# Kernel optimization log

Measured on AMD Instinct MI355X. Metric: run time of the kernel, lower is better.

Reference implementation:

```python
import jax, jax.numpy as jnp
import numpy as np

D = 256      # hidden_size
H = 4        # num_attention_heads
DH = D // H  # dim per head = 64
L = 4        # num_hidden_layers
M = 266      # nb_features = int(64 * ln(64))
S = 4096     # seq len / max_position_embeddings
B = 4
LN_EPS = 1e-12


def layer_norm(x, g, b, eps=LN_EPS):
    mu = jnp.mean(x, -1, keepdims=True)
    var = jnp.var(x, -1, keepdims=True)
    return (x - mu) / jnp.sqrt(var + eps) * g + b


def softmax_kernel(x, proj, is_query, eps=1e-4):
    # x: [b,h,s,d], proj: [m,d] -> phi(x): [b,h,s,m] (FAVOR+ positive features)
    d = x.shape[-1]
    m = proj.shape[0]
    dn = d ** -0.25
    ratio = m ** -0.5
    dash = jnp.einsum('bhsd,md->bhsm', x, proj) * dn
    diag = jnp.sum(x * x, -1, keepdims=True) * 0.5 * (dn * dn)
    if is_query:
        stab = jnp.max(dash, -1, keepdims=True)  # per-query stabilizer
    else:
        stab = jnp.max(dash)  # global stabilizer for keys
    return ratio * (jnp.exp(dash - diag - stab) + eps)


def favor_attention(x, proj, Wq, bq, Wk, bk, Wv, bv, Wo, bo):
    b, s, d = x.shape
    split = lambda t: t.reshape(b, s, H, DH).transpose(0, 2, 1, 3)  # [b,h,s,dh]
    q = split(x @ Wq + bq)
    k = split(x @ Wk + bk)
    v = split(x @ Wv + bv)
    qp = softmax_kernel(q, proj, True)   # [b,h,s,m]
    kp = softmax_kernel(k, proj, False)  # [b,h,s,m]
    ksum = kp.sum(axis=2)                                  # [b,h,m]
    d_inv = 1.0 / jnp.einsum('bhsm,bhm->bhs', qp, ksum)    # normalizer
    ctx = jnp.einsum('bhsm,bhse->bhme', kp, v)             # [b,h,m,dh]
    out = jnp.einsum('bhsm,bhme,bhs->bhse', qp, ctx, d_inv)
    out = out.transpose(0, 2, 1, 3).reshape(b, s, d)
    return out @ Wo + bo


def _forward(input_embs, attention_mask, pos_emb, ln_g, ln_b, proj,
             Wq, bq, Wk, bk, Wv, bv, Wo, bo, ln1_g, ln1_b,
             W1, b1, W2, b2, ln2_g, ln2_b, p1_w, p1_b, p2_w, p2_b):
    b, s, d = input_embs.shape
    x = input_embs + pos_emb[:s][None]
    x = layer_norm(x, ln_g, ln_b)  # dropout is identity at eval
    for i in range(L):
        x = x + favor_attention(layer_norm(x, ln1_g[i], ln1_b[i]), proj[i],
                                Wq[i], bq[i], Wk[i], bk[i], Wv[i], bv[i], Wo[i], bo[i])
        h = layer_norm(x, ln2_g[i], ln2_b[i])
        x = x + (jax.nn.gelu(h @ W1[i] + b1[i]) @ W2[i] + b2[i])
    # AttentionPooling
    e = jnp.tanh(x @ p1_w + p1_b)
    alpha = jnp.exp(e @ p2_w + p2_b)            # [b,s,1]
    alpha = alpha * attention_mask[..., None]
    alpha = alpha / (jnp.sum(alpha, 1, keepdims=True) + 1e-8)
    return jnp.einsum('bsd,bs->bd', x, alpha[..., 0])


def setup_inputs() -> dict:
    key = jax.random.key(0)
    ks = iter(jax.random.split(key, 32))
    std = 0.02
    nrm = lambda shape: jax.random.normal(next(ks), shape, jnp.float32)
    return {
        'input_embs': nrm((B, S, D)),
        'attention_mask': jnp.ones((B, S), jnp.float32),
        'pos_emb': nrm((S, D)) * std,
        'ln_g': jnp.ones((D,), jnp.float32), 'ln_b': jnp.zeros((D,), jnp.float32),
        'proj': nrm((L, M, DH)),
        'Wq': nrm((L, D, D)) * std, 'bq': jnp.zeros((L, D), jnp.float32),
        'Wk': nrm((L, D, D)) * std, 'bk': jnp.zeros((L, D), jnp.float32),
        'Wv': nrm((L, D, D)) * std, 'bv': jnp.zeros((L, D), jnp.float32),
        'Wo': nrm((L, D, D)) * std, 'bo': jnp.zeros((L, D), jnp.float32),
        'ln1_g': jnp.ones((L, D), jnp.float32), 'ln1_b': jnp.zeros((L, D), jnp.float32),
        'W1': nrm((L, D, 4 * D)) * std, 'b1': jnp.zeros((L, 4 * D), jnp.float32),
        'W2': nrm((L, 4 * D, D)) * std, 'b2': jnp.zeros((L, D), jnp.float32),
        'ln2_g': jnp.ones((L, D), jnp.float32), 'ln2_b': jnp.zeros((L, D), jnp.float32),
        'p1_w': nrm((D, D)) * std, 'p1_b': jnp.zeros((D,), jnp.float32),
        'p2_w': nrm((D, 1)) * std, 'p2_b': jnp.zeros((1,), jnp.float32),
    }


def reference(input_embs, attention_mask, pos_emb, ln_g, ln_b, proj,
              Wq, bq, Wk, bk, Wv, bv, Wo, bo, ln1_g, ln1_b,
              W1, b1, W2, b2, ln2_g, ln2_b, p1_w, p1_b, p2_w, p2_b):
    return _forward(input_embs, attention_mask, pos_emb, ln_g, ln_b, proj,
                    Wq, bq, Wk, bk, Wv, bv, Wo, bo, ln1_g, ln1_b,
                    W1, b1, W2, b2, ln2_g, ln2_b, p1_w, p1_b, p2_w, p2_b)
```

## Files before the change

### kernel.cpp

```cpp
#include <hip/hip_runtime.h>
#include <math.h>


#define WS_ALIGN(x) (((x) + 255) & ~(size_t)255)

#define DN 0.35355339059327373f
#define DIAGC 0.0625f
#define RATIO 0.06131393394849658f
#define FEPS 1e-4f

typedef __attribute__((__ext_vector_type__(8))) __bf16 bf16x8;
typedef __attribute__((__ext_vector_type__(4))) float f32x4;

__device__ __forceinline__ float wredsum(float v) {
    v += __shfl_xor(v, 32); v += __shfl_xor(v, 16); v += __shfl_xor(v, 8);
    v += __shfl_xor(v, 4);  v += __shfl_xor(v, 2);  v += __shfl_xor(v, 1);
    return v;
}
__device__ __forceinline__ float wredmax(float v) {
    v = fmaxf(v, __shfl_xor(v, 32)); v = fmaxf(v, __shfl_xor(v, 16));
    v = fmaxf(v, __shfl_xor(v, 8));  v = fmaxf(v, __shfl_xor(v, 4));
    v = fmaxf(v, __shfl_xor(v, 2));  v = fmaxf(v, __shfl_xor(v, 1));
    return v;
}

__device__ __forceinline__ unsigned short f2bf(float f) {
    unsigned u = __builtin_bit_cast(unsigned, f);
    return (unsigned short)((u + 0x7fffu + ((u >> 16) & 1u)) >> 16);
}
__device__ __forceinline__ float blo(unsigned x) { return __builtin_bit_cast(float, x << 16); }
__device__ __forceinline__ float bhi(unsigned x) { return __builtin_bit_cast(float, x & 0xffff0000u); }
__device__ __forceinline__ float sumsq8(uint4 u) {
    float s = 0.f;
    s += blo(u.x)*blo(u.x) + bhi(u.x)*bhi(u.x);
    s += blo(u.y)*blo(u.y) + bhi(u.y)*bhi(u.y);
    s += blo(u.z)*blo(u.z) + bhi(u.z)*bhi(u.z);
    s += blo(u.w)*blo(u.w) + bhi(u.w)*bhi(u.w);
    return s;
}
__device__ __forceinline__ unsigned pack2(float a, float b) {
    return (unsigned)f2bf(a) | ((unsigned)f2bf(b) << 16);
}

__device__ __forceinline__ void gload_lds16(const unsigned short* g, unsigned short* lds) {
    __builtin_amdgcn_global_load_lds(
        (const __attribute__((address_space(1))) unsigned int*)g,
        (__attribute__((address_space(3))) unsigned int*)lds, 16, 0, 0);
}

__global__ __launch_bounds__(256) void add_ln2_kernel(
    const float* __restrict__ in, const float* __restrict__ pos,
    const float* __restrict__ g0, const float* __restrict__ b0,
    const float* __restrict__ g1, const float* __restrict__ b1,
    float* __restrict__ xout, unsigned short* __restrict__ hout)
{
    int row = blockIdx.x, t = threadIdx.x;
    __shared__ float sred[4];
    float v = in[(size_t)row * 256 + t] + pos[(size_t)(row & 4095) * 256 + t];
    float s = wredsum(v);
    if ((t & 63) == 0) sred[t >> 6] = s;
    __syncthreads();
    float mean = (sred[0] + sred[1] + sred[2] + sred[3]) * (1.0f / 256.0f);
    float d = v - mean;
    __syncthreads();
    float sq = wredsum(d * d);
    if ((t & 63) == 0) sred[t >> 6] = sq;
    __syncthreads();
    float var = (sred[0] + sred[1] + sred[2] + sred[3]) * (1.0f / 256.0f);
    float y1 = d * rsqrtf(var + 1e-12f) * g0[t] + b0[t];
    xout[(size_t)row * 256 + t] = y1;
    __syncthreads();
    float s1 = wredsum(y1);
    if ((t & 63) == 0) sred[t >> 6] = s1;
    __syncthreads();
    float mean1 = (sred[0] + sred[1] + sred[2] + sred[3]) * (1.0f / 256.0f);
    float d1 = y1 - mean1;
    __syncthreads();
    float sq1 = wredsum(d1 * d1);
    if ((t & 63) == 0) sred[t >> 6] = sq1;
    __syncthreads();
    float var1 = (sred[0] + sred[1] + sred[2] + sred[3]) * (1.0f / 256.0f);
    hout[(size_t)row * 256 + t] = f2bf(d1 * rsqrtf(var1 + 1e-12f) * g1[t] + b1[t]);
}

__global__ __launch_bounds__(256) void cast_transpose_kernel(
    const float* __restrict__ in, unsigned short* __restrict__ out, int R, int C)
{
    __shared__ float tile[32][33];
    size_t zo = (size_t)blockIdx.z * R * C;
    int c0 = blockIdx.x * 32, r0 = blockIdx.y * 32;
    int t = threadIdx.x, tc = t & 31, tr = t >> 5;
#pragma unroll
    for (int j = 0; j < 4; j++)
        tile[tr + j * 8][tc] = in[zo + (size_t)(r0 + tr + j * 8) * C + c0 + tc];
    __syncthreads();
#pragma unroll
    for (int j = 0; j < 4; j++) {
        int cc = tr + j * 8, rr = tc;
        out[zo + (size_t)(c0 + cc) * R + r0 + rr] = f2bf(tile[rr][cc]);
    }
}

__global__ __launch_bounds__(256) void cast_transpose4_kernel(
    const float* __restrict__ i0, const float* __restrict__ i1,
    const float* __restrict__ i2, const float* __restrict__ i3,
    unsigned short* __restrict__ o0, unsigned short* __restrict__ o1,
    unsigned short* __restrict__ o2, unsigned short* __restrict__ o3)
{
    __shared__ float tile[32][33];
    int z = blockIdx.z;
    int which = z >> 2, layer = z & 3;
    const float* in = (which == 0) ? i0 : (which == 1) ? i1 : (which == 2) ? i2 : i3;
    unsigned short* out = (which == 0) ? o0 : (which == 1) ? o1 : (which == 2) ? o2 : o3;
    size_t zo = (size_t)layer * 65536;
    int c0 = blockIdx.x * 32, r0 = blockIdx.y * 32;
    int t = threadIdx.x, tc = t & 31, tr = t >> 5;
#pragma unroll
    for (int j = 0; j < 4; j++)
        tile[tr + j * 8][tc] = in[zo + (size_t)(r0 + tr + j * 8) * 256 + c0 + tc];
    __syncthreads();
#pragma unroll
    for (int j = 0; j < 4; j++) {
        int cc = tr + j * 8, rr = tc;
        out[zo + (size_t)(c0 + cc) * 256 + r0 + rr] = f2bf(tile[rr][cc]);
    }
}

__global__ __launch_bounds__(256) void cast_row_kernel(
    const float4* __restrict__ in, ushort4* __restrict__ out, int n4)
{
    int i = blockIdx.x * 256 + threadIdx.x;
    if (i >= n4) return;
    float4 v = in[i];
    ushort4 o; o.x = f2bf(v.x); o.y = f2bf(v.y); o.z = f2bf(v.z); o.w = f2bf(v.w);
    out[i] = o;
}

__global__ __launch_bounds__(256) void ctx_cast_kernel(
    const float* __restrict__ ctxT, unsigned short* __restrict__ ctxbf)
{
    int idx = blockIdx.x * 256 + threadIdx.x;
    int row = idx / 36;
    int c = idx - row * 36;
    int m = c * 8;
    uint4 pk = {0, 0, 0, 0};
    if (m < 272) {
        const float* src = ctxT + (size_t)row * 272 + m;
        float4 f0 = *(const float4*)(src);
        float4 f1 = *(const float4*)(src + 4);
        pk.x = pack2(f0.x, f0.y); pk.y = pack2(f0.z, f0.w);
        pk.z = pack2(f1.x, f1.y); pk.w = pack2(f1.z, f1.w);
    }
    *(uint4*)(ctxbf + (size_t)row * 288 + c * 8) = pk;
}

__global__ __launch_bounds__(256) void qkv_kernel(
    const unsigned short* __restrict__ A,
    const unsigned short* __restrict__ Wqt, const unsigned short* __restrict__ Wkt,
    const unsigned short* __restrict__ Wvt,
    const float* __restrict__ bq, const float* __restrict__ bk, const float* __restrict__ bv,
    unsigned short* __restrict__ qbf, unsigned short* __restrict__ kbf,
    unsigned short* __restrict__ vT)
{
    __shared__ uint4 As[128][5];
    __shared__ uint4 Bs[64][5];
    const int K = 256;
    int t = threadIdx.x;
    int bm = blockIdx.y * 128, bn = blockIdx.x * 64;
    int grp = bn >> 8, lbn = bn & 255;
    const unsigned short* Bt = (grp == 0) ? Wqt : (grp == 1) ? Wkt : Wvt;
    const float* bias = (grp == 0) ? bq : (grp == 1) ? bk : bv;
    int w = t >> 6, l = t & 63, lm16 = l & 15, quad = l >> 4;
    int ar = t >> 1, ak = (t & 1) * 16;
    int br = t >> 2, bk2 = (t & 3) * 8;
    const unsigned short* Ab = A + (size_t)(bm + ar) * K + ak;
    const unsigned short* Bb = Bt + (size_t)(lbn + br) * K + bk2;
    f32x4 acc[2][4] = {};
    for (int k0 = 0; k0 < K; k0 += 32) {
        uint4 a0 = *(const uint4*)(Ab + k0);
        uint4 a1 = *(const uint4*)(Ab + k0 + 8);
        uint4 b0 = *(const uint4*)(Bb + k0);
        __syncthreads();
        As[ar][(ak >> 3)] = a0; As[ar][(ak >> 3) + 1] = a1;
        Bs[br][bk2 >> 3] = b0;
        __syncthreads();
        bf16x8 af[2], bfr[4];
        af[0] = *(const bf16x8*)&As[w * 32 + lm16][quad];
        af[1] = *(const bf16x8*)&As[w * 32 + 16 + lm16][quad];
#pragma unroll
        for (int j = 0; j < 4; j++) bfr[j] = *(const bf16x8*)&Bs[j * 16 + lm16][quad];
#pragma unroll
        for (int i = 0; i < 2; i++)
#pragma unroll
            for (int j = 0; j < 4; j++)
                acc[i][j] = __builtin_amdgcn_mfma_f32_16x16x32_bf16(af[i], bfr[j], acc[i][j], 0, 0, 0);
    }
#pragma unroll
    for (int i = 0; i < 2; i++)
#pragma unroll
        for (int j = 0; j < 4; j++) {
            int lcol = lbn + j * 16 + lm16;
            float bs = bias[lcol];
            int h = lcol >> 6, e = lcol & 63;
#pragma unroll
            for (int r = 0; r < 4; r++) {
                int row = bm + w * 32 + i * 16 + quad * 4 + r;
                int b = row >> 12, s = row & 4095;
                float v = acc[i][j][r] + bs;
                if (grp == 0)
                    qbf[((size_t)((b << 2) + h) * 4096 + s) * 64 + e] = f2bf(v);
                else if (grp == 1)
                    kbf[((size_t)((b << 2) + h) * 4096 + s) * 64 + e] = f2bf(v);
                else
                    vT[((size_t)((b << 2) + h) * 64 + e) * 4096 + s] = f2bf(v);
            }
        }
}

__global__ __launch_bounds__(256) void ffn1_kernel(
    const unsigned short* __restrict__ A, const unsigned short* __restrict__ Bt,
    const float* __restrict__ bias, unsigned short* __restrict__ Cb, int N, int K)
{
    __shared__ uint4 As[128][5];
    __shared__ uint4 Bs[64][5];
    int t = threadIdx.x;
    int bm = blockIdx.y * 128, bn = blockIdx.x * 64;
    int w = t >> 6, l = t & 63, lm16 = l & 15, quad = l >> 4;
    int ar = t >> 1, ak = (t & 1) * 16;
    int br = t >> 2, bk = (t & 3) * 8;
    const unsigned short* Ab = A + (size_t)(bm + ar) * K + ak;
    const unsigned short* Bb = Bt + (size_t)(bn + br) * K + bk;
    f32x4 acc[2][4] = {};
    for (int k0 = 0; k0 < K; k0 += 32) {
        uint4 a0 = *(const uint4*)(Ab + k0);
        uint4 a1 = *(const uint4*)(Ab + k0 + 8);
        uint4 b0 = *(const uint4*)(Bb + k0);
        __syncthreads();
        As[ar][(ak >> 3)] = a0; As[ar][(ak >> 3) + 1] = a1;
        Bs[br][bk >> 3] = b0;
        __syncthreads();
        bf16x8 af[2], bfr[4];
        af[0] = *(const bf16x8*)&As[w * 32 + lm16][quad];
        af[1] = *(const bf16x8*)&As[w * 32 + 16 + lm16][quad];
#pragma unroll
        for (int j = 0; j < 4; j++) bfr[j] = *(const bf16x8*)&Bs[j * 16 + lm16][quad];
#pragma unroll
        for (int i = 0; i < 2; i++)
#pragma unroll
            for (int j = 0; j < 4; j++)
                acc[i][j] = __builtin_amdgcn_mfma_f32_16x16x32_bf16(af[i], bfr[j], acc[i][j], 0, 0, 0);
    }
#pragma unroll
    for (int i = 0; i < 2; i++)
#pragma unroll
        for (int j = 0; j < 4; j++) {
            int col = bn + j * 16 + lm16;
            float bsv = bias[col];
#pragma unroll
            for (int r = 0; r < 4; r++) {
                int row = bm + w * 32 + i * 16 + quad * 4 + r;
                float v = acc[i][j][r] + bsv;
                float inner = 0.7978845608028654f * (v + 0.044715f * v * v * v);
                float gl = 0.5f * v * (1.0f + tanhf(inner));
                Cb[(size_t)row * N + col] = f2bf(gl);
            }
        }
}

template <int EPI>
__global__ __launch_bounds__(512) void gemm_fullrow_kernel(
    const unsigned short* __restrict__ A, const unsigned short* __restrict__ Bt,
    const float* __restrict__ bias, float* __restrict__ xio,
    const float* __restrict__ lng, const float* __restrict__ lnb,
    unsigned short* __restrict__ outb,
    const float* __restrict__ p2w, const float* __restrict__ p2b,
    const float* __restrict__ mask, float* __restrict__ alphab, int K)
{
    __shared__ uint4 As4[64][5];
    __shared__ uint4 Bs4[256][5];
    __shared__ float red[8][64];
    int t = threadIdx.x;
    int bm = blockIdx.x * 64;
    int w = t >> 6, l = t & 63, lm16 = l & 15, quad = l >> 4;
    int br = t >> 2, bj = t & 3;
    f32x4 acc[4][2] = {};
    for (int k0 = 0; k0 < K; k0 += 32) {
        uint4 a = {0, 0, 0, 0};
        if (t < 256) a = *(const uint4*)(A + (size_t)(bm + (t >> 2)) * K + k0 + (t & 3) * 8);
        uint4 b0 = *(const uint4*)(Bt + (size_t)br * K + k0 + bj * 8);
        uint4 b1 = *(const uint4*)(Bt + (size_t)(br + 128) * K + k0 + bj * 8);
        __syncthreads();
        if (t < 256) As4[t >> 2][t & 3] = a;
        Bs4[br][bj] = b0;
        Bs4[br + 128][bj] = b1;
        __syncthreads();
        bf16x8 af[4], bfv[2];
#pragma unroll
        for (int i = 0; i < 4; i++) af[i] = *(const bf16x8*)&As4[i * 16 + lm16][quad];
#pragma unroll
        for (int j = 0; j < 2; j++) bfv[j] = *(const bf16x8*)&Bs4[w * 32 + j * 16 + lm16][quad];
#pragma unroll
        for (int i = 0; i < 4; i++)
#pragma unroll
            for (int j = 0; j < 2; j++)
                acc[i][j] = __builtin_amdgcn_mfma_f32_16x16x32_bf16(af[i], bfv[j], acc[i][j], 0, 0, 0);
    }
    int colbase = w * 32;
    if (EPI == 2) {
        float rs[4][4] = {};
#pragma unroll
        for (int j = 0; j < 2; j++) {
            int col = colbase + j * 16 + lm16;
            float bs = bias[col], pw = p2w[col];
#pragma unroll
            for (int i = 0; i < 4; i++)
#pragma unroll
                for (int r = 0; r < 4; r++)
                    rs[i][r] += tanhf(acc[i][j][r] + bs) * pw;
        }
#pragma unroll
        for (int m2 = 1; m2 <= 8; m2 <<= 1)
#pragma unroll
            for (int i = 0; i < 4; i++)
#pragma unroll
                for (int r = 0; r < 4; r++) rs[i][r] += __shfl_xor(rs[i][r], m2);
        __syncthreads();
        if (lm16 == 0) {
#pragma unroll
            for (int i = 0; i < 4; i++)
#pragma unroll
                for (int r = 0; r < 4; r++) red[w][i * 16 + quad * 4 + r] = rs[i][r];
        }
        __syncthreads();
        if (t < 64) {
            float sc = p2b[0];
#pragma unroll
            for (int ww = 0; ww < 8; ww++) sc += red[ww][t];
            int row = bm + t;
            alphab[row] = expf(sc) * mask[row];
        }
        return;
    }
    float rs[4][4] = {};
#pragma unroll
    for (int j = 0; j < 2; j++) {
        int col = colbase + j * 16 + lm16;
        float bs = bias[col];
#pragma unroll
        for (int i = 0; i < 4; i++)
#pragma unroll
            for (int r = 0; r < 4; r++) {
                int row = bm + i * 16 + quad * 4 + r;
                float v = acc[i][j][r] + bs + xio[(size_t)row * 256 + col];
                acc[i][j][r] = v;
                rs[i][r] += v;
            }
    }
    float mean[4][4], rstd[4][4];
    if (EPI == 0) {
#pragma unroll
        for (int m2 = 1; m2 <= 8; m2 <<= 1)
#pragma unroll
            for (int i = 0; i < 4; i++)
#pragma unroll
                for (int r = 0; r < 4; r++) rs[i][r] += __shfl_xor(rs[i][r], m2);
        __syncthreads();
        if (lm16 == 0) {
#pragma unroll
            for (int i = 0; i < 4; i++)
#pragma unroll
                for (int r = 0; r < 4; r++) red[w][i * 16 + quad * 4 + r] = rs[i][r];
        }
        __syncthreads();
        float vs[4][4] = {};
#pragma unroll
        for (int i = 0; i < 4; i++)
#pragma unroll
            for (int r = 0; r < 4; r++) {
                int rr = i * 16 + quad * 4 + r;
                float s = 0.f;
#pragma unroll
                for (int ww = 0; ww < 8; ww++) s += red[ww][rr];
                mean[i][r] = s * (1.0f / 256.0f);
            }
#pragma unroll
        for (int j = 0; j < 2; j++)
#pragma unroll
            for (int i = 0; i < 4; i++)
#pragma unroll
                for (int r = 0; r < 4; r++) {
                    float d = acc[i][j][r] - mean[i][r];
                    vs[i][r] += d * d;
                }
#pragma unroll
        for (int m2 = 1; m2 <= 8; m2 <<= 1)
#pragma unroll
            for (int i = 0; i < 4; i++)
#pragma unroll
                for (int r = 0; r < 4; r++) vs[i][r] += __shfl_xor(vs[i][r], m2);
        __syncthreads();
        if (lm16 == 0) {
#pragma unroll
            for (int i = 0; i < 4; i++)
#pragma unroll
                for (int r = 0; r < 4; r++) red[w][i * 16 + quad * 4 + r] = vs[i][r];
        }
        __syncthreads();
#pragma unroll
        for (int i = 0; i < 4; i++)
#pragma unroll
            for (int r = 0; r < 4; r++) {
                int rr = i * 16 + quad * 4 + r;
                float s = 0.f;
#pragma unroll
                for (int ww = 0; ww < 8; ww++) s += red[ww][rr];
                rstd[i][r] = rsqrtf(s * (1.0f / 256.0f) + 1e-12f);
            }
    }
#pragma unroll
    for (int j = 0; j < 2; j++) {
        int col = colbase + j * 16 + lm16;
        float g  = (EPI == 0) ? lng[col] : 0.f;
        float bb = (EPI == 0) ? lnb[col] : 0.f;
#pragma unroll
        for (int i = 0; i < 4; i++)
#pragma unroll
            for (int r = 0; r < 4; r++) {
                int row = bm + i * 16 + quad * 4 + r;
                float v = acc[i][j][r];
                xio[(size_t)row * 256 + col] = v;
                float y = (EPI == 0) ? ((v - mean[i][r]) * rstd[i][r] * g + bb) : v;
                outb[(size_t)row * 256 + col] = f2bf(y);
            }
    }
}

#define ZERO_FLOATS 282880
__global__ __launch_bounds__(256) void phi_kmax_kernel(
    const unsigned short* __restrict__ kbf, const unsigned short* __restrict__ projbf,
    float* __restrict__ pmax, float* __restrict__ zbase)
{
    __shared__ uint4 As[64][9];
    __shared__ uint4 Bs[272][9];
    __shared__ float diag_s[64];
    __shared__ float sred[4];
    int t = threadIdx.x;
    int s0 = blockIdx.x * 64;
    int bh = blockIdx.y;
    {
        int bid = blockIdx.y * 64 + blockIdx.x;
        for (int i = bid * 256 + t; i < ZERO_FLOATS; i += 1024 * 256) zbase[i] = 0.f;
    }
    {
        int arow = t >> 2, akoff = (t & 3) * 16;
        const uint4* ga = (const uint4*)(kbf + ((size_t)bh * 4096 + s0 + arow) * 64 + akoff);
        uint4 u0 = ga[0], u1 = ga[1];
        As[arow][(akoff >> 3)] = u0; As[arow][(akoff >> 3) + 1] = u1;
        float ss = sumsq8(u0) + sumsq8(u1);
        ss += __shfl_xor(ss, 1); ss += __shfl_xor(ss, 2);
        if ((t & 3) == 0) diag_s[arow] = DIAGC * ss;
        uint4 zero = {0, 0, 0, 0};
        for (int row = t; row < 272; row += 256) {
            const uint4* gp = (const uint4*)(projbf + (size_t)row * 64);
            bool bv = row < 266;
#pragma unroll
            for (int i2 = 0; i2 < 8; i2++) Bs[row][i2] = bv ? gp[i2] : zero;
        }
    }
    __syncthreads();
    int w = t >> 6, l = t & 63, lm16 = l & 15, quad = l >> 4;
    f32x4 acc[17] = {};
#pragma unroll
    for (int ks = 0; ks < 2; ks++) {
        bf16x8 af = *(const bf16x8*)&As[w * 16 + lm16][ks * 4 + quad];
#pragma unroll
        for (int j = 0; j < 17; j++) {
            bf16x8 bfv = *(const bf16x8*)&Bs[j * 16 + lm16][ks * 4 + quad];
            acc[j] = __builtin_amdgcn_mfma_f32_16x16x32_bf16(af, bfv, acc[j], 0, 0, 0);
        }
    }
    int rloc = w * 16 + quad * 4;
    float kmax = -1e30f;
#pragma unroll
    for (int j = 0; j < 17; j++) {
        int m = j * 16 + lm16;
        bool valid = m < 266;
#pragma unroll
        for (int r = 0; r < 4; r++)
            if (valid) kmax = fmaxf(kmax, acc[j][r] * DN - diag_s[rloc + r]);
    }
    kmax = wredmax(kmax);
    if (l == 0) sred[w] = kmax;
    __syncthreads();
    if (t == 0)
        pmax[(size_t)bh * 64 + blockIdx.x] =
            fmaxf(fmaxf(sred[0], sred[1]), fmaxf(sred[2], sred[3]));
}

__global__ __launch_bounds__(256) void ctx_fused_kernel(
    const unsigned short* __restrict__ kbf, const unsigned short* __restrict__ vT,
    const unsigned short* __restrict__ projbf, const float* __restrict__ pmax,
    float* __restrict__ ksum, float* __restrict__ ctxT)
{
    __shared__ uint4 Ap[64][9];
    __shared__ uint4 Ks[64][9];
    __shared__ uint4 Vs[64][9];
    __shared__ unsigned short kp_s[64][72];
    __shared__ float diag_s[64];
    __shared__ float sred2[4];
    int t = threadIdx.x;
    int m0 = blockIdx.x * 64;
    int bh = blockIdx.y;
    int sb = blockIdx.z * 512;
    int w = t >> 6, l = t & 63, lm16 = l & 15, quad = l >> 4;
    {
        int row = t >> 2, koff = (t & 3) * 16;
        uint4 zero = {0, 0, 0, 0};
        bool bv = (m0 + row) < 266;
        const uint4* gp = (const uint4*)(projbf + (size_t)(m0 + row) * 64 + koff);
        Ap[row][(koff >> 3)] = bv ? gp[0] : zero;
        Ap[row][(koff >> 3) + 1] = bv ? gp[1] : zero;
    }
    float pm = -1e30f;
    for (int i = t; i < 1024; i += 256) pm = fmaxf(pm, pmax[i]);
    pm = wredmax(pm);
    if (l == 0) sred2[w] = pm;
    __syncthreads();
    float st = fmaxf(fmaxf(sred2[0], sred2[1]), fmaxf(sred2[2], sred2[3]));
    f32x4 accc[4] = {};
    float ksacc[4] = {0.f, 0.f, 0.f, 0.f};
    int srow = t >> 2, skoff = (t & 3) * 16;
    for (int kc = 0; kc < 8; kc++) {
        int sc = sb + kc * 64;
        const uint4* gk = (const uint4*)(kbf + ((size_t)bh * 4096 + sc + srow) * 64 + skoff);
        uint4 k0 = gk[0], k1 = gk[1];
        const uint4* gv = (const uint4*)(vT + ((size_t)bh * 64 + srow) * 4096 + sc + skoff);
        uint4 v0 = gv[0], v1 = gv[1];
        __syncthreads();
        Ks[srow][(skoff >> 3)] = k0; Ks[srow][(skoff >> 3) + 1] = k1;
        Vs[srow][(skoff >> 3)] = v0; Vs[srow][(skoff >> 3) + 1] = v1;
        float ss = sumsq8(k0) + sumsq8(k1);
        ss += __shfl_xor(ss, 1); ss += __shfl_xor(ss, 2);
        if ((t & 3) == 0) diag_s[srow] = DIAGC * ss;
        __syncthreads();
        f32x4 accd[4] = {};
#pragma unroll
        for (int ks = 0; ks < 2; ks++) {
            bf16x8 af = *(const bf16x8*)&Ap[w * 16 + lm16][ks * 4 + quad];
#pragma unroll
            for (int j = 0; j < 4; j++) {
                bf16x8 bfv = *(const bf16x8*)&Ks[j * 16 + lm16][ks * 4 + quad];
                accd[j] = __builtin_amdgcn_mfma_f32_16x16x32_bf16(af, bfv, accd[j], 0, 0, 0);
            }
        }
        int mbase = m0 + w * 16 + quad * 4;
#pragma unroll
        for (int j = 0; j < 4; j++) {
            int s_loc = j * 16 + lm16;
            float dgv = diag_s[s_loc];
#pragma unroll
            for (int r = 0; r < 4; r++) {
                float v = accd[j][r] * DN - dgv;
                float e = (mbase + r < 266) ? RATIO * (__expf(v - st) + FEPS) : 0.f;
                kp_s[w * 16 + quad * 4 + r][s_loc] = f2bf(e);
                ksacc[r] += e;
            }
        }
        __syncthreads();
#pragma unroll
        for (int ks = 0; ks < 2; ks++) {
            bf16x8 af = *(const bf16x8*)&Vs[w * 16 + lm16][ks * 4 + quad];
#pragma unroll
            for (int jt = 0; jt < 4; jt++) {
                bf16x8 bfv = *(const bf16x8*)&kp_s[jt * 16 + lm16][ks * 32 + quad * 8];
                accc[jt] = __builtin_amdgcn_mfma_f32_16x16x32_bf16(af, bfv, accc[jt], 0, 0, 0);
            }
        }
    }
#pragma unroll
    for (int r = 0; r < 4; r++) {
        float v = ksacc[r];
        v += __shfl_xor(v, 1); v += __shfl_xor(v, 2);
        v += __shfl_xor(v, 4); v += __shfl_xor(v, 8);
        if (lm16 == 0) {
            int m = m0 + w * 16 + quad * 4 + r;
            if (m < 272) atomicAdd(&ksum[bh * 272 + m], v);
        }
    }
#pragma unroll
    for (int jt = 0; jt < 4; jt++) {
        int m = m0 + jt * 16 + lm16;
        if (m >= 272) continue;
#pragma unroll
        for (int r = 0; r < 4; r++) {
            int e = w * 16 + quad * 4 + r;
            atomicAdd(&ctxT[((size_t)bh * 64 + e) * 272 + m], accc[jt][r]);
        }
    }
}

__global__ __launch_bounds__(256) void phi_q_attn_kernel(
    const unsigned short* __restrict__ qbf, const unsigned short* __restrict__ projbf,
    const float* __restrict__ ksum, const unsigned short* __restrict__ ctxbf,
    unsigned short* __restrict__ abf)
{
    __shared__ uint4 uA[1152];
    __shared__ uint4 bufB[272][8];
    __shared__ float diag_s[64];
    __shared__ float den_s[64];
    int t = threadIdx.x;
    int s0 = blockIdx.x * 64;
    int bh = blockIdx.y;
    int w = t >> 6, l = t & 63, lm16 = l & 15, quad = l >> 4;
    uint4 (*bufA)[9] = (uint4(*)[9])uA;
    {
        int arow = t >> 2, akoff = (t & 3) * 16;
        const uint4* ga = (const uint4*)(qbf + ((size_t)bh * 4096 + s0 + arow) * 64 + akoff);
        uint4 u0 = ga[0], u1 = ga[1];
        bufA[arow][(akoff >> 3)] = u0; bufA[arow][(akoff >> 3) + 1] = u1;
        float ss = sumsq8(u0) + sumsq8(u1);
        ss += __shfl_xor(ss, 1); ss += __shfl_xor(ss, 2);
        if ((t & 3) == 0) diag_s[arow] = DIAGC * ss;
        uint4 zero = {0, 0, 0, 0};
        for (int row = t; row < 272; row += 256) {
            const uint4* gp = (const uint4*)(projbf + (size_t)row * 64);
            bool bv = row < 266;
            int sw = row & 7;
#pragma unroll
            for (int c = 0; c < 8; c++) bufB[row][c ^ sw] = bv ? gp[c] : zero;
        }
    }
    float ksv[17];
#pragma unroll
    for (int j = 0; j < 17; j++) ksv[j] = ksum[bh * 272 + j * 16 + lm16];
    __syncthreads();
    f32x4 acc[17] = {};
#pragma unroll
    for (int ks = 0; ks < 2; ks++) {
        bf16x8 af = *(const bf16x8*)&bufA[w * 16 + lm16][ks * 4 + quad];
#pragma unroll
        for (int j = 0; j < 17; j++) {
            bf16x8 bfv = *(const bf16x8*)&bufB[j * 16 + lm16][(ks * 4 + quad) ^ (lm16 & 7)];
            acc[j] = __builtin_amdgcn_mfma_f32_16x16x32_bf16(af, bfv, acc[j], 0, 0, 0);
        }
    }
    int rloc = w * 16 + quad * 4;
    float dg[4];
#pragma unroll
    for (int r = 0; r < 4; r++) dg[r] = diag_s[rloc + r];
    float vmax[4] = {-1e30f, -1e30f, -1e30f, -1e30f};
#pragma unroll
    for (int j = 0; j < 17; j++) {
        int m = j * 16 + lm16;
        bool valid = m < 266;
#pragma unroll
        for (int r = 0; r < 4; r++) {
            float v = acc[j][r] * DN - dg[r];
            acc[j][r] = v;
            if (valid) vmax[r] = fmaxf(vmax[r], v);
        }
    }
#pragma unroll
    for (int m2 = 1; m2 <= 8; m2 <<= 1)
#pragma unroll
        for (int r = 0; r < 4; r++) vmax[r] = fmaxf(vmax[r], __shfl_xor(vmax[r], m2));
    __syncthreads();
    unsigned short* ctxs = (unsigned short*)uA;
    const unsigned short* ctxg = ctxbf + (size_t)bh * 64 * 288;
    for (int i = w; i < 18; i += 4)
        gload_lds16(ctxg + i * 512 + l * 8, ctxs + i * 512);
    unsigned short* qp_s = (unsigned short*)bufB;
    float den[4] = {0.f, 0.f, 0.f, 0.f};
#pragma unroll
    for (int j = 0; j < 17; j++) {
        int m = j * 16 + lm16;
        bool valid = m < 266;
#pragma unroll
        for (int r = 0; r < 4; r++) {
            float e = valid ? RATIO * (__expf(acc[j][r] - vmax[r]) + FEPS) : 0.f;
            qp_s[(rloc + r) * 272 + m] = f2bf(e);
            den[r] += e * ksv[j];
        }
    }
#pragma unroll
    for (int m2 = 1; m2 <= 8; m2 <<= 1)
#pragma unroll
        for (int r = 0; r < 4; r++) den[r] += __shfl_xor(den[r], m2);
    if (lm16 == 0) {
#pragma unroll
        for (int r = 0; r < 4; r++) den_s[rloc + r] = den[r];
    }
    bf16x8 paf[9];
#pragma unroll
    for (int kk = 0; kk < 9; kk++)
        paf[kk] = *(const bf16x8*)&qp_s[(w * 16 + lm16) * 272 + kk * 32 + quad * 8];
    __syncthreads();
    int b = bh >> 2, h = bh & 3;
    f32x4 oacc[4] = {};
#pragma unroll
    for (int qd = 0; qd < 4; qd++) {
        const unsigned short* cs = ctxs + (qd & 1) * 4608;
#pragma unroll
        for (int kk = 0; kk < 9; kk++) {
            bf16x8 bfv = *(const bf16x8*)&cs[lm16 * 288 + kk * 32 + quad * 8];
            oacc[qd] = __builtin_amdgcn_mfma_f32_16x16x32_bf16(paf[kk], bfv, oacc[qd], 0, 0, 0);
        }
        if (qd < 3) {
            __syncthreads();
            if (qd < 2) {
                for (int i = w; i < 9; i += 4)
                    gload_lds16(ctxg + (qd + 2) * 4608 + i * 512 + l * 8,
                                ctxs + (qd & 1) * 4608 + i * 512);
            }
        }
    }
#pragma unroll
    for (int qd = 0; qd < 4; qd++) {
        int e = qd * 16 + lm16;
#pragma unroll
        for (int r = 0; r < 4; r++) {
            int sl = rloc + r;
            abf[((size_t)(b * 4096 + s0 + sl)) * 256 + h * 64 + e] = f2bf(oacc[qd][r] / den_s[sl]);
        }
    }
}

__global__ __launch_bounds__(256) void pool_denom_kernel(
    const float* __restrict__ alpha, float* __restrict__ denomb)
{
    __shared__ float sred[4];
    int b = blockIdx.x, t = threadIdx.x;
    float p = 0.f;
    for (int s = t; s < 4096; s += 256) p += alpha[b * 4096 + s];
    p = wredsum(p);
    if ((t & 63) == 0) sred[t >> 6] = p;
    __syncthreads();
    if (t == 0) denomb[b] = sred[0] + sred[1] + sred[2] + sred[3] + 1e-8f;
}

__global__ __launch_bounds__(256) void pool_out_kernel(
    const float* __restrict__ x, const float* __restrict__ alpha,
    const float* __restrict__ denomb, float* __restrict__ out)
{
    int b = blockIdx.x, chunk = blockIdx.y, t = threadIdx.x;
    float inv = 1.0f / denomb[b];
    float acc = 0.f;
    int s0 = chunk * 128;
    for (int s = s0; s < s0 + 128; s++)
        acc += x[((size_t)(b << 12) + s) * 256 + t] * alpha[(b << 12) + s];
    atomicAdd(&out[b * 256 + t], acc * inv);
}

extern "C" void kernel_launch(void* const* d_in, const int* in_sizes, int n_in,
                              void* d_out, int out_size, void* d_ws, size_t ws_size,
                              hipStream_t stream)
{
    const float* input_embs = (const float*)d_in[0];
    const float* mask  = (const float*)d_in[1];
    const float* pos   = (const float*)d_in[2];
    const float* ln_g  = (const float*)d_in[3];
    const float* ln_b  = (const float*)d_in[4];
    const float* proj  = (const float*)d_in[5];
    const float* Wq = (const float*)d_in[6];  const float* bq = (const float*)d_in[7];
    const float* Wk = (const float*)d_in[8];  const float* bk = (const float*)d_in[9];
    const float* Wv = (const float*)d_in[10]; const float* bv = (const float*)d_in[11];
    const float* Wo = (const float*)d_in[12]; const float* bo = (const float*)d_in[13];
    const float* ln1g = (const float*)d_in[14]; const float* ln1b = (const float*)d_in[15];
    const float* W1 = (const float*)d_in[16]; const float* b1 = (const float*)d_in[17];
    const float* W2 = (const float*)d_in[18]; const float* b2 = (const float*)d_in[19];
    const float* ln2g = (const float*)d_in[20]; const float* ln2b = (const float*)d_in[21];
    const float* p1w = (const float*)d_in[22]; const float* p1b = (const float*)d_in[23];
    const float* p2w = (const float*)d_in[24]; const float* p2b = (const float*)d_in[25];
    float* out = (float*)d_out;
    char* ws = (char*)d_ws;

    size_t off = 0;
    auto alloc = [&](size_t bytes) { size_t o = off; off += WS_ALIGN(bytes); return o; };
    float* xbuf = (float*)(ws + alloc(16384ull * 256 * 4));
    unsigned short* hbf = (unsigned short*)(ws + alloc(16384ull * 256 * 2));
    unsigned short* qbf = (unsigned short*)(ws + alloc(16384ull * 256 * 2));
    unsigned short* kbf = (unsigned short*)(ws + alloc(16384ull * 256 * 2));
    unsigned short* vT  = (unsigned short*)(ws + alloc(16384ull * 256 * 2));
    unsigned short* midbf = (unsigned short*)(ws + alloc(16384ull * 1024 * 2));
    size_t ksum_off = alloc(16ull * 272 * 4);
    float* ksum = (float*)(ws + ksum_off);
    float* ctxT = (float*)(ws + alloc(16ull * 64 * 272 * 4));
    float* pmaxb = (float*)(ws + alloc(1024ull * 4));
    float* alphab = (float*)(ws + alloc(16384ull * 4));
    float* pdenom = (float*)(ws + alloc(256));
    unsigned short* Wqt = (unsigned short*)(ws + alloc(4ull * 65536 * 2));
    unsigned short* Wkt = (unsigned short*)(ws + alloc(4ull * 65536 * 2));
    unsigned short* Wvt = (unsigned short*)(ws + alloc(4ull * 65536 * 2));
    unsigned short* Wot = (unsigned short*)(ws + alloc(4ull * 65536 * 2));
    unsigned short* W1t = (unsigned short*)(ws + alloc(4ull * 262144 * 2));
    unsigned short* W2t = (unsigned short*)(ws + alloc(4ull * 262144 * 2));
    unsigned short* projbf = (unsigned short*)(ws + alloc(4ull * 17024 * 2));
    unsigned short* p1t = (unsigned short*)(ws + alloc(65536ull * 2));
    unsigned short* ctxbf = (unsigned short*)(ws + alloc(16ull * 64 * 288 * 2));
    unsigned short* abf = hbf;

    cast_transpose4_kernel<<<dim3(8, 8, 16), 256, 0, stream>>>(Wq, Wk, Wv, Wo, Wqt, Wkt, Wvt, Wot);
    cast_transpose_kernel<<<dim3(32, 8, 4), 256, 0, stream>>>(W1, W1t, 256, 1024);
    cast_transpose_kernel<<<dim3(8, 32, 4), 256, 0, stream>>>(W2, W2t, 1024, 256);
    cast_transpose_kernel<<<dim3(8, 8, 1), 256, 0, stream>>>(p1w, p1t, 256, 256);
    cast_row_kernel<<<67, 256, 0, stream>>>((const float4*)proj, (ushort4*)projbf, 17024);

    add_ln2_kernel<<<16384, 256, 0, stream>>>(input_embs, pos, ln_g, ln_b, ln1g, ln1b, xbuf, hbf);

    for (int i = 0; i < 4; i++) {
        const unsigned short* pj = projbf + (size_t)i * 17024;
        qkv_kernel<<<dim3(12, 128), 256, 0, stream>>>(hbf,
            Wqt + (size_t)i * 65536, Wkt + (size_t)i * 65536, Wvt + (size_t)i * 65536,
            bq + i * 256, bk + i * 256, bv + i * 256, qbf, kbf, vT);
        phi_kmax_kernel<<<dim3(64, 16), 256, 0, stream>>>(kbf, pj, pmaxb, ksum);
        ctx_fused_kernel<<<dim3(5, 16, 8), 256, 0, stream>>>(kbf, vT, pj, pmaxb, ksum, ctxT);
        ctx_cast_kernel<<<144, 256, 0, stream>>>(ctxT, ctxbf);
        phi_q_attn_kernel<<<dim3(64, 16), 256, 0, stream>>>(qbf, pj, ksum, ctxbf, abf);
        gemm_fullrow_kernel<0><<<256, 512, 0, stream>>>(abf, Wot + (size_t)i * 65536,
            bo + i * 256, xbuf, ln2g + i * 256, ln2b + i * 256, hbf,
            nullptr, nullptr, nullptr, nullptr, 256);
        ffn1_kernel<<<dim3(16, 128), 256, 0, stream>>>(hbf, W1t + (size_t)i * 262144,
            b1 + i * 1024, midbf, 1024, 256);
        if (i < 3)
            gemm_fullrow_kernel<0><<<256, 512, 0, stream>>>(midbf, W2t + (size_t)i * 262144,
                b2 + i * 256, xbuf, ln1g + (i + 1) * 256, ln1b + (i + 1) * 256, hbf,
                nullptr, nullptr, nullptr, nullptr, 1024);
        else
            gemm_fullrow_kernel<1><<<256, 512, 0, stream>>>(midbf, W2t + (size_t)i * 262144,
                b2 + i * 256, xbuf, nullptr, nullptr, hbf,
                nullptr, nullptr, nullptr, nullptr, 1024);
    }

    gemm_fullrow_kernel<2><<<256, 512, 0, stream>>>(hbf, p1t, p1b, nullptr, nullptr, nullptr,
        nullptr, p2w, p2b, mask, alphab, 256);
    pool_denom_kernel<<<4, 256, 0, stream>>>(alphab, pdenom);
    hipMemsetAsync(d_out, 0, (size_t)out_size * sizeof(float), stream);
    pool_out_kernel<<<dim3(4, 32), 256, 0, stream>>>(xbuf, alphab, pdenom, out);
}
```

Baseline: 863.3 us.

## Double-buffer GEMM tiles with direct global-to-LDS loads and XOR swizzle

The qkv, ffn1 and full-row GEMM kernels now stage tiles straight from global memory into LDS with a direct-to-LDS load helper. Two LDS buffers let the next K-slice load while the current one runs through MFMA, and one barrier per iteration replaces two. The LDS layout uses an XOR swizzle instead of padding to avoid bank conflicts. The projection matrix is cast to bf16 once into a zero-padded 272-row layout per layer, so the phi kernels can copy it into swizzled LDS the same way without bounds checks. This costs more LDS per block, which may lower occupancy, and the swizzle indices must match between writers and readers.

```diff
diff --git a/kernel.cpp b/kernel.cpp
--- a/kernel.cpp
+++ b/kernel.cpp
@@ -126,14 +126,22 @@
     }
 }
 
-__global__ __launch_bounds__(256) void cast_row_kernel(
-    const float4* __restrict__ in, ushort4* __restrict__ out, int n4)
-{
-    int i = blockIdx.x * 256 + threadIdx.x;
-    if (i >= n4) return;
-    float4 v = in[i];
-    ushort4 o; o.x = f2bf(v.x); o.y = f2bf(v.y); o.z = f2bf(v.z); o.w = f2bf(v.w);
-    out[i] = o;
+__global__ __launch_bounds__(256) void proj_cast_kernel(
+    const float* __restrict__ proj, unsigned short* __restrict__ projbf)
+{
+    int idx = blockIdx.x * 256 + threadIdx.x;
+    if (idx >= 10240) return;
+    int li = idx / 2560; int rem = idx - li * 2560;
+    int m = rem >> 3; int c = rem & 7;
+    uint4 pk = {0, 0, 0, 0};
+    if (m < 266) {
+        const float* src = proj + ((size_t)li * 266 + m) * 64 + c * 8;
+        float4 f0 = *(const float4*)(src);
+        float4 f1 = *(const float4*)(src + 4);
+        pk.x = pack2(f0.x, f0.y); pk.y = pack2(f0.z, f0.w);
+        pk.z = pack2(f1.x, f1.y); pk.w = pack2(f1.z, f1.w);
+    }
+    *(uint4*)(projbf + (size_t)idx * 8) = pk;
 }
 
 __global__ __launch_bounds__(256) void ctx_cast_kernel(
@@ -162,8 +170,8 @@
     unsigned short* __restrict__ qbf, unsigned short* __restrict__ kbf,
     unsigned short* __restrict__ vT)
 {
-    __shared__ uint4 As[128][5];
-    __shared__ uint4 Bs[64][5];
+    __shared__ unsigned short As[2][4096];
+    __shared__ unsigned short Bs[2][2048];
     const int K = 256;
     int t = threadIdx.x;
     int bm = blockIdx.y * 128, bn = blockIdx.x * 64;
@@ -171,29 +179,33 @@
     const unsigned short* Bt = (grp == 0) ? Wqt : (grp == 1) ? Wkt : Wvt;
     const float* bias = (grp == 0) ? bq : (grp == 1) ? bk : bv;
     int w = t >> 6, l = t & 63, lm16 = l & 15, quad = l >> 4;
-    int ar = t >> 1, ak = (t & 1) * 16;
-    int br = t >> 2, bk2 = (t & 3) * 8;
-    const unsigned short* Ab = A + (size_t)(bm + ar) * K + ak;
-    const unsigned short* Bb = Bt + (size_t)(lbn + br) * K + bk2;
+    int gc8 = ((l & 3) ^ ((l >> 3) & 3)) * 8;
+    int rc8 = (quad ^ ((lm16 >> 1) & 3)) * 8;
+    const unsigned short* pa0 = A + (size_t)(bm + w * 16 + (l >> 2)) * K + gc8;
+    const unsigned short* pa1 = pa0 + (size_t)64 * K;
+    const unsigned short* pb0 = Bt + (size_t)(lbn + w * 16 + (l >> 2)) * K + gc8;
+    auto stage = [&](int buf, int k0) {
+        gload_lds16(pa0 + k0, &As[buf][w * 512]);
+        gload_lds16(pa1 + k0, &As[buf][w * 512 + 2048]);
+        gload_lds16(pb0 + k0, &Bs[buf][w * 512]);
+    };
+    stage(0, 0);
     f32x4 acc[2][4] = {};
-    for (int k0 = 0; k0 < K; k0 += 32) {
-        uint4 a0 = *(const uint4*)(Ab + k0);
-        uint4 a1 = *(const uint4*)(Ab + k0 + 8);
-        uint4 b0 = *(const uint4*)(Bb + k0);
-        __syncthreads();
-        As[ar][(ak >> 3)] = a0; As[ar][(ak >> 3) + 1] = a1;
-        Bs[br][bk2 >> 3] = b0;
-        __syncthreads();
+    __syncthreads();
+    for (int kt = 0; kt < 8; ++kt) {
+        int cur = kt & 1;
+        if (kt < 7) stage(cur ^ 1, (kt + 1) * 32);
         bf16x8 af[2], bfr[4];
-        af[0] = *(const bf16x8*)&As[w * 32 + lm16][quad];
-        af[1] = *(const bf16x8*)&As[w * 32 + 16 + lm16][quad];
-#pragma unroll
-        for (int j = 0; j < 4; j++) bfr[j] = *(const bf16x8*)&Bs[j * 16 + lm16][quad];
+        af[0] = *(const bf16x8*)&As[cur][(w * 32 + lm16) * 32 + rc8];
+        af[1] = *(const bf16x8*)&As[cur][(w * 32 + 16 + lm16) * 32 + rc8];
+#pragma unroll
+        for (int j = 0; j < 4; j++) bfr[j] = *(const bf16x8*)&Bs[cur][(j * 16 + lm16) * 32 + rc8];
 #pragma unroll
         for (int i = 0; i < 2; i++)
 #pragma unroll
             for (int j = 0; j < 4; j++)
                 acc[i][j] = __builtin_amdgcn_mfma_f32_16x16x32_bf16(af[i], bfr[j], acc[i][j], 0, 0, 0);
+        __syncthreads();
     }
 #pragma unroll
     for (int i = 0; i < 2; i++)
@@ -221,34 +233,39 @@
     const unsigned short* __restrict__ A, const unsigned short* __restrict__ Bt,
     const float* __restrict__ bias, unsigned short* __restrict__ Cb, int N, int K)
 {
-    __shared__ uint4 As[128][5];
-    __shared__ uint4 Bs[64][5];
+    __shared__ unsigned short As[2][4096];
+    __shared__ unsigned short Bs[2][2048];
     int t = threadIdx.x;
     int bm = blockIdx.y * 128, bn = blockIdx.x * 64;
     int w = t >> 6, l = t & 63, lm16 = l & 15, quad = l >> 4;
-    int ar = t >> 1, ak = (t & 1) * 16;
-    int br = t >> 2, bk = (t & 3) * 8;
-    const unsigned short* Ab = A + (size_t)(bm + ar) * K + ak;
-    const unsigned short* Bb = Bt + (size_t)(bn + br) * K + bk;
+    int gc8 = ((l & 3) ^ ((l >> 3) & 3)) * 8;
+    int rc8 = (quad ^ ((lm16 >> 1) & 3)) * 8;
+    const unsigned short* pa0 = A + (size_t)(bm + w * 16 + (l >> 2)) * K + gc8;
+    const unsigned short* pa1 = pa0 + (size_t)64 * K;
+    const unsigned short* pb0 = Bt + (size_t)(bn + w * 16 + (l >> 2)) * K + gc8;
+    auto stage = [&](int buf, int k0) {
+        gload_lds16(pa0 + k0, &As[buf][w * 512]);
+        gload_lds16(pa1 + k0, &As[buf][w * 512 + 2048]);
+        gload_lds16(pb0 + k0, &Bs[buf][w * 512]);
+    };
+    stage(0, 0);
     f32x4 acc[2][4] = {};
-    for (int k0 = 0; k0 < K; k0 += 32) {
-        uint4 a0 = *(const uint4*)(Ab + k0);
-        uint4 a1 = *(const uint4*)(Ab + k0 + 8);
-        uint4 b0 = *(const uint4*)(Bb + k0);
-        __syncthreads();
-        As[ar][(ak >> 3)] = a0; As[ar][(ak >> 3) + 1] = a1;
-        Bs[br][bk >> 3] = b0;
-        __syncthreads();
+    __syncthreads();
+    int nt = K >> 5;
+    for (int kt = 0; kt < nt; ++kt) {
+        int cur = kt & 1;
+        if (kt < nt - 1) stage(cur ^ 1, (kt + 1) * 32);
         bf16x8 af[2], bfr[4];
-        af[0] = *(const bf16x8*)&As[w * 32 + lm16][quad];
-        af[1] = *(const bf16x8*)&As[w * 32 + 16 + lm16][quad];
-#pragma unroll
-        for (int j = 0; j < 4; j++) bfr[j] = *(const bf16x8*)&Bs[j * 16 + lm16][quad];
+        af[0] = *(const bf16x8*)&As[cur][(w * 32 + lm16) * 32 + rc8];
+        af[1] = *(const bf16x8*)&As[cur][(w * 32 + 16 + lm16) * 32 + rc8];
+#pragma unroll
+        for (int j = 0; j < 4; j++) bfr[j] = *(const bf16x8*)&Bs[cur][(j * 16 + lm16) * 32 + rc8];
 #pragma unroll
         for (int i = 0; i < 2; i++)
 #pragma unroll
             for (int j = 0; j < 4; j++)
                 acc[i][j] = __builtin_amdgcn_mfma_f32_16x16x32_bf16(af[i], bfr[j], acc[i][j], 0, 0, 0);
+        __syncthreads();
     }
 #pragma unroll
     for (int i = 0; i < 2; i++)
@@ -276,34 +293,40 @@
     const float* __restrict__ p2w, const float* __restrict__ p2b,
     const float* __restrict__ mask, float* __restrict__ alphab, int K)
 {
-    __shared__ uint4 As4[64][5];
-    __shared__ uint4 Bs4[256][5];
-    __shared__ float red[8][64];
+    __shared__ unsigned short As2[2][2048];
+    __shared__ unsigned short Bs2[2][8192];
+    float (*red)[64] = (float (*)[64])As2;
     int t = threadIdx.x;
     int bm = blockIdx.x * 64;
     int w = t >> 6, l = t & 63, lm16 = l & 15, quad = l >> 4;
-    int br = t >> 2, bj = t & 3;
+    int gc8 = ((l & 3) ^ ((l >> 3) & 3)) * 8;
+    int rc8 = (quad ^ ((lm16 >> 1) & 3)) * 8;
+    const unsigned short* pa = A + (size_t)(bm + (w & 3) * 16 + (l >> 2)) * K + gc8;
+    const unsigned short* pb0 = Bt + (size_t)(w * 16 + (l >> 2)) * K + gc8;
+    const unsigned short* pb1 = pb0 + (size_t)128 * K;
+    auto stage = [&](int buf, int k0) {
+        if (w < 4) gload_lds16(pa + k0, &As2[buf][w * 512]);
+        gload_lds16(pb0 + k0, &Bs2[buf][w * 512]);
+        gload_lds16(pb1 + k0, &Bs2[buf][w * 512 + 4096]);
+    };
+    stage(0, 0);
     f32x4 acc[4][2] = {};
-    for (int k0 = 0; k0 < K; k0 += 32) {
-        uint4 a = {0, 0, 0, 0};
-        if (t < 256) a = *(const uint4*)(A + (size_t)(bm + (t >> 2)) * K + k0 + (t & 3) * 8);
-        uint4 b0 = *(const uint4*)(Bt + (size_t)br * K + k0 + bj * 8);
-        uint4 b1 = *(const uint4*)(Bt + (size_t)(br + 128) * K + k0 + bj * 8);
-        __syncthreads();
-        if (t < 256) As4[t >> 2][t & 3] = a;
-        Bs4[br][bj] = b0;
-        Bs4[br + 128][bj] = b1;
-        __syncthreads();
+    __syncthreads();
+    int nt = K >> 5;
+    for (int kt = 0; kt < nt; ++kt) {
+        int cur = kt & 1;
+        if (kt < nt - 1) stage(cur ^ 1, (kt + 1) * 32);
         bf16x8 af[4], bfv[2];
 #pragma unroll
-        for (int i = 0; i < 4; i++) af[i] = *(const bf16x8*)&As4[i * 16 + lm16][quad];
-#pragma unroll
-        for (int j = 0; j < 2; j++) bfv[j] = *(const bf16x8*)&Bs4[w * 32 + j * 16 + lm16][quad];
+        for (int i = 0; i < 4; i++) af[i] = *(const bf16x8*)&As2[cur][(i * 16 + lm16) * 32 + rc8];
+#pragma unroll
+        for (int j = 0; j < 2; j++) bfv[j] = *(const bf16x8*)&Bs2[cur][(w * 32 + j * 16 + lm16) * 32 + rc8];
 #pragma unroll
         for (int i = 0; i < 4; i++)
 #pragma unroll
             for (int j = 0; j < 2; j++)
                 acc[i][j] = __builtin_amdgcn_mfma_f32_16x16x32_bf16(af[i], bfv[j], acc[i][j], 0, 0, 0);
+        __syncthreads();
     }
     int colbase = w * 32;
     if (EPI == 2) {
@@ -441,12 +464,13 @@
     float* __restrict__ pmax, float* __restrict__ zbase)
 {
     __shared__ uint4 As[64][9];
-    __shared__ uint4 Bs[272][9];
+    __shared__ uint4 Bs[272][8];
     __shared__ float diag_s[64];
     __shared__ float sred[4];
     int t = threadIdx.x;
     int s0 = blockIdx.x * 64;
     int bh = blockIdx.y;
+    int w = t >> 6, l = t & 63, lm16 = l & 15, quad = l >> 4;
     {
         int bid = blockIdx.y * 64 + blockIdx.x;
         for (int i = bid * 256 + t; i < ZERO_FLOATS; i += 1024 * 256) zbase[i] = 0.f;
@@ -459,23 +483,22 @@
         float ss = sumsq8(u0) + sumsq8(u1);
         ss += __shfl_xor(ss, 1); ss += __shfl_xor(ss, 2);
         if ((t & 3) == 0) diag_s[arow] = DIAGC * ss;
-        uint4 zero = {0, 0, 0, 0};
-        for (int row = t; row < 272; row += 256) {
-            const uint4* gp = (const uint4*)(projbf + (size_t)row * 64);
-            bool bv = row < 266;
-#pragma unroll
-            for (int i2 = 0; i2 < 8; i2++) Bs[row][i2] = bv ? gp[i2] : zero;
-        }
-    }
-    __syncthreads();
-    int w = t >> 6, l = t & 63, lm16 = l & 15, quad = l >> 4;
+    }
+    {
+        unsigned short* Pl = (unsigned short*)Bs;
+        int gcp8 = ((l & 7) ^ ((l >> 3) & 7)) * 8;
+        const unsigned short* ps = projbf + (size_t)(l >> 3) * 64 + gcp8;
+        for (int i = w; i < 34; i += 4)
+            gload_lds16(ps + (size_t)i * 512, Pl + i * 512);
+    }
+    __syncthreads();
     f32x4 acc[17] = {};
 #pragma unroll
     for (int ks = 0; ks < 2; ks++) {
         bf16x8 af = *(const bf16x8*)&As[w * 16 + lm16][ks * 4 + quad];
 #pragma unroll
         for (int j = 0; j < 17; j++) {
-            bf16x8 bfv = *(const bf16x8*)&Bs[j * 16 + lm16][ks * 4 + quad];
+            bf16x8 bfv = *(const bf16x8*)&Bs[j * 16 + lm16][(ks * 4 + quad) ^ (lm16 & 7)];
             acc[j] = __builtin_amdgcn_mfma_f32_16x16x32_bf16(af, bfv, acc[j], 0, 0, 0);
         }
     }
@@ -502,7 +525,7 @@
     const unsigned short* __restrict__ projbf, const float* __restrict__ pmax,
     float* __restrict__ ksum, float* __restrict__ ctxT)
 {
-    __shared__ uint4 Ap[64][9];
+    __shared__ uint4 Ap[64][8];
     __shared__ uint4 Ks[64][9];
     __shared__ uint4 Vs[64][9];
     __shared__ unsigned short kp_s[64][72];
@@ -514,12 +537,11 @@
     int sb = blockIdx.z * 512;
     int w = t >> 6, l = t & 63, lm16 = l & 15, quad = l >> 4;
     {
-        int row = t >> 2, koff = (t & 3) * 16;
-        uint4 zero = {0, 0, 0, 0};
-        bool bv = (m0 + row) < 266;
-        const uint4* gp = (const uint4*)(projbf + (size_t)(m0 + row) * 64 + koff);
-        Ap[row][(koff >> 3)] = bv ? gp[0] : zero;
-        Ap[row][(koff >> 3) + 1] = bv ? gp[1] : zero;
+        unsigned short* Pl = (unsigned short*)Ap;
+        int gcp8 = ((l & 7) ^ ((l >> 3) & 7)) * 8;
+        const unsigned short* ps = projbf + (size_t)(m0 + (l >> 3)) * 64 + gcp8;
+        for (int i = w; i < 8; i += 4)
+            gload_lds16(ps + (size_t)i * 512, Pl + i * 512);
     }
     float pm = -1e30f;
     for (int i = t; i < 1024; i += 256) pm = fmaxf(pm, pmax[i]);
@@ -546,7 +568,7 @@
         f32x4 accd[4] = {};
 #pragma unroll
         for (int ks = 0; ks < 2; ks++) {
-            bf16x8 af = *(const bf16x8*)&Ap[w * 16 + lm16][ks * 4 + quad];
+            bf16x8 af = *(const bf16x8*)&Ap[w * 16 + lm16][(ks * 4 + quad) ^ (lm16 & 7)];
 #pragma unroll
             for (int j = 0; j < 4; j++) {
                 bf16x8 bfv = *(const bf16x8*)&Ks[j * 16 + lm16][ks * 4 + quad];
@@ -621,14 +643,13 @@
         float ss = sumsq8(u0) + sumsq8(u1);
         ss += __shfl_xor(ss, 1); ss += __shfl_xor(ss, 2);
         if ((t & 3) == 0) diag_s[arow] = DIAGC * ss;
-        uint4 zero = {0, 0, 0, 0};
-        for (int row = t; row < 272; row += 256) {
-            const uint4* gp = (const uint4*)(projbf + (size_t)row * 64);
-            bool bv = row < 266;
-            int sw = row & 7;
-#pragma unroll
-            for (int c = 0; c < 8; c++) bufB[row][c ^ sw] = bv ? gp[c] : zero;
-        }
+    }
+    {
+        unsigned short* Pl = (unsigned short*)bufB;
+        int gcp8 = ((l & 7) ^ ((l >> 3) & 7)) * 8;
+        const unsigned short* ps = projbf + (size_t)(l >> 3) * 64 + gcp8;
+        for (int i = w; i < 34; i += 4)
+            gload_lds16(ps + (size_t)i * 512, Pl + i * 512);
     }
     float ksv[17];
 #pragma unroll
@@ -794,7 +815,7 @@
     unsigned short* Wot = (unsigned short*)(ws + alloc(4ull * 65536 * 2));
     unsigned short* W1t = (unsigned short*)(ws + alloc(4ull * 262144 * 2));
     unsigned short* W2t = (unsigned short*)(ws + alloc(4ull * 262144 * 2));
-    unsigned short* projbf = (unsigned short*)(ws + alloc(4ull * 17024 * 2));
+    unsigned short* projbf = (unsigned short*)(ws + alloc(4ull * 20480 * 2));
     unsigned short* p1t = (unsigned short*)(ws + alloc(65536ull * 2));
     unsigned short* ctxbf = (unsigned short*)(ws + alloc(16ull * 64 * 288 * 2));
     unsigned short* abf = hbf;
@@ -803,12 +824,12 @@
     cast_transpose_kernel<<<dim3(32, 8, 4), 256, 0, stream>>>(W1, W1t, 256, 1024);
     cast_transpose_kernel<<<dim3(8, 32, 4), 256, 0, stream>>>(W2, W2t, 1024, 256);
     cast_transpose_kernel<<<dim3(8, 8, 1), 256, 0, stream>>>(p1w, p1t, 256, 256);
-    cast_row_kernel<<<67, 256, 0, stream>>>((const float4*)proj, (ushort4*)projbf, 17024);
+    proj_cast_kernel<<<40, 256, 0, stream>>>(proj, projbf);
 
     add_ln2_kernel<<<16384, 256, 0, stream>>>(input_embs, pos, ln_g, ln_b, ln1g, ln1b, xbuf, hbf);
 
     for (int i = 0; i < 4; i++) {
-        const unsigned short* pj = projbf + (size_t)i * 17024;
+        const unsigned short* pj = projbf + (size_t)i * 20480;
         qkv_kernel<<<dim3(12, 128), 256, 0, stream>>>(hbf,
             Wqt + (size_t)i * 65536, Wkt + (size_t)i * 65536, Wvt + (size_t)i * 65536,
             bq + i * 256, bk + i * 256, bv + i * 256, qbf, kbf, vT);
```

Measured after the change: 801.1 us. 7.2% less time.
